# Kernel optimization log

Hardware: AMD Instinct MI355X
Metric: run time of the kernel (lower is better)

## Reference

```python
import jax, jax.numpy as jnp
import numpy as np

EMBED_DIM = 2048
NUM_HEADS = 16
HEAD_DIM = EMBED_DIM // NUM_HEADS  # 128
BLOCK_SIZE = 16
NUM_BLOCKS = 256  # max_seq_len 4096 / block_size 16
B = 64
T = 1  # single decode token per sequence (loop indexes k[i, 0, 0])


def setup_inputs() -> dict:
    key = jax.random.key(0)
    ks = jax.random.split(key, 12)
    w = 0.02
    return {
        "x": jax.random.normal(ks[0], (B, T, EMBED_DIM), jnp.float32),
        "k_cache": jax.random.normal(ks[1], (B, NUM_BLOCKS, BLOCK_SIZE, HEAD_DIM), jnp.float32),
        "v_cache": jax.random.normal(ks[2], (B, NUM_BLOCKS, BLOCK_SIZE, HEAD_DIM), jnp.float32),
        "cache_positions": jax.random.randint(ks[3], (B,), 0, NUM_BLOCKS * BLOCK_SIZE, jnp.int32),
        "Wq": jax.random.normal(ks[4], (EMBED_DIM, EMBED_DIM), jnp.float32) * w,
        "bq": jax.random.normal(ks[5], (EMBED_DIM,), jnp.float32) * w,
        "Wk": jax.random.normal(ks[6], (EMBED_DIM, HEAD_DIM), jnp.float32) * w,
        "bk": jax.random.normal(ks[7], (HEAD_DIM,), jnp.float32) * w,
        "Wv": jax.random.normal(ks[8], (EMBED_DIM, HEAD_DIM), jnp.float32) * w,
        "bv": jax.random.normal(ks[9], (HEAD_DIM,), jnp.float32) * w,
        "Wo": jax.random.normal(ks[10], (EMBED_DIM, EMBED_DIM), jnp.float32) * w,
        "bo": jax.random.normal(ks[11], (EMBED_DIM,), jnp.float32) * w,
    }


def reference(x, k_cache, v_cache, cache_positions, Wq, bq, Wk, bk, Wv, bv, Wo, bo):
    b, t, c = x.shape  # t == 1 (decode)
    hd = Wk.shape[1]
    h = c // hd
    scale = 1.0 / jnp.sqrt(jnp.asarray(hd, x.dtype))

    q = (x @ Wq + bq).reshape(b, t, h, hd)          # [B,1,H,hd]
    k_new = (x @ Wk + bk)[:, 0, :]                  # [B,hd] single KV head
    v_new = (x @ Wv + bv)[:, 0, :]                  # [B,hd]

    # Paged scatter: flatten (num_blocks, block_size) -> S slots; write new token at pos.
    s = k_cache.shape[1] * k_cache.shape[2]
    bidx = jnp.arange(b)
    kc = k_cache.reshape(b, s, hd).at[bidx, cache_positions].set(k_new)  # [B,S,hd]
    vc = v_cache.reshape(b, s, hd).at[bidx, cache_positions].set(v_new)

    # MQA: single KV head broadcast across H query heads. NOTE: softmax over the
    # FULL flattened cache (no validity mask), matching the original module.
    scores = jnp.einsum("bthd,bsd->bhts", q, kc) * scale   # [B,H,1,S]
    attn = jax.nn.softmax(scores, axis=-1)
    out = jnp.einsum("bhts,bsd->bthd", attn, vc).reshape(b, t, c)
    return out @ Wo + bo
```

## Files before the change

### kernel.cpp

```cpp
#include <hip/hip_runtime.h>
#include <math.h>

#define EMBED   2048
#define NHEADS  16
#define HD      128
#define S_TOT   4096
#define BATCH   64

typedef __attribute__((ext_vector_type(8))) short short8v;
typedef __attribute__((ext_vector_type(4))) short short4v;
typedef __attribute__((ext_vector_type(2))) short short2v;
typedef __attribute__((ext_vector_type(4))) float floatx4;

__device__ __forceinline__ unsigned short f2bf(float f) {
    unsigned u = __builtin_bit_cast(unsigned, f);
    u += 0x7fffu + ((u >> 16) & 1u);
    return (unsigned short)(u >> 16);
}

template <int CTRL>
__device__ __forceinline__ float dppf(float x) {
    int r = __builtin_amdgcn_mov_dpp(__builtin_bit_cast(int, x), CTRL, 0xF, 0xF, false);
    return __builtin_bit_cast(float, r);
}
__device__ __forceinline__ float rowmax16(float v) {
    v = fmaxf(v, dppf<0x121>(v));
    v = fmaxf(v, dppf<0x122>(v));
    v = fmaxf(v, dppf<0x124>(v));
    v = fmaxf(v, dppf<0x128>(v));
    return v;
}
__device__ __forceinline__ float rowsum16(float v) {
    v += dppf<0x121>(v);
    v += dppf<0x122>(v);
    v += dppf<0x124>(v);
    v += dppf<0x128>(v);
    return v;
}

__launch_bounds__(256)
__global__ void k1_qkv(const float* __restrict__ x,
                       const float* __restrict__ Wq, const float* __restrict__ bq,
                       const float* __restrict__ Wk, const float* __restrict__ bk,
                       const float* __restrict__ Wv, const float* __restrict__ bv,
                       float* __restrict__ qbuf, float* __restrict__ knew,
                       float* __restrict__ vnew) {
    const int tx = threadIdx.x & 31;
    const int ty = threadIdx.x >> 5;
    const int nt = blockIdx.x;
    const int kc = blockIdx.y;
    const int k0 = kc * 256;
    const int col0 = nt * 32;

    const float* W; const float* bias; float* out; int ldW;
    int cbase;
    if (col0 < 2048)       { W = Wq; bias = bq; out = qbuf; ldW = 2048; cbase = col0; }
    else if (col0 < 2176)  { W = Wk; bias = bk; out = knew; ldW = 128;  cbase = col0 - 2048; }
    else                   { W = Wv; bias = bv; out = vnew; ldW = 128;  cbase = col0 - 2176; }
    const int col = cbase + tx;

    __shared__ __align__(16) float xs[64][68];

    float acc[8] = {0, 0, 0, 0, 0, 0, 0, 0};

    for (int sub = 0; sub < 4; ++sub) {
        const int kb = k0 + sub * 64;
        #pragma unroll
        for (int i = 0; i < 4; ++i) {
            int c = threadIdx.x + i * 256;
            int r = c >> 4;
            int cc = (c & 15) << 2;
            float4 v = *(const float4*)(x + (size_t)r * EMBED + kb + cc);
            *(float4*)&xs[r][cc] = v;
        }
        __syncthreads();
        #pragma unroll
        for (int kk = 0; kk < 64; kk += 4) {
            float w0 = W[(size_t)(kb + kk + 0) * ldW + col];
            float w1 = W[(size_t)(kb + kk + 1) * ldW + col];
            float w2 = W[(size_t)(kb + kk + 2) * ldW + col];
            float w3 = W[(size_t)(kb + kk + 3) * ldW + col];
            #pragma unroll
            for (int j = 0; j < 8; ++j) {
                int m = ty + (j << 3);
                float4 xv = *(const float4*)&xs[m][kk];
                acc[j] = fmaf(xv.x, w0, acc[j]);
                acc[j] = fmaf(xv.y, w1, acc[j]);
                acc[j] = fmaf(xv.z, w2, acc[j]);
                acc[j] = fmaf(xv.w, w3, acc[j]);
            }
        }
        __syncthreads();
    }
    if (kc == 0) {
        float b = bias[col];
        #pragma unroll
        for (int j = 0; j < 8; ++j) acc[j] += b;
    }
    const int ldO = (ldW == 2048) ? 2048 : 128;
    #pragma unroll
    for (int j = 0; j < 8; ++j)
        atomicAdd(&out[(size_t)(ty + (j << 3)) * ldO + col], acc[j]);
}

__launch_bounds__(256)
__global__ void k2_attn(const float* __restrict__ qbuf,
                        const float* __restrict__ kcache,
                        const float* __restrict__ vcache,
                        const float* __restrict__ knew,
                        const float* __restrict__ vnew,
                        const int* __restrict__ cpos,
                        float* __restrict__ part_o,
                        float* __restrict__ part_ml)
{
    const int b = blockIdx.y;
    const int chunk = blockIdx.x;
    const int nch = gridDim.x;
    const int C = nch * 4;
    const int spw = S_TOT / C;
    const int nst = spw >> 5;
    const int tid = threadIdx.x;
    const int w = tid >> 6;
    const int lane = tid & 63;
    const int quad = lane >> 4;
    const int lm = lane & 15;
    const int pos = cpos[b];

    __shared__ __align__(16) short qs[16 * 136];
    __shared__ __align__(16) short vsh[4][64 * 40];
    __shared__ __align__(16) short psh[4][16 * 40];

    {
        const int h = tid >> 4, d0 = (tid & 15) << 3;
        const float* src = qbuf + (size_t)b * EMBED + h * HD + d0;
        float4 a = *(const float4*)src;
        float4 c = *(const float4*)(src + 4);
        const float s = 0.08838834764831845f;
        short8v pk;
        pk[0] = f2bf(a.x * s); pk[1] = f2bf(a.y * s);
        pk[2] = f2bf(a.z * s); pk[3] = f2bf(a.w * s);
        pk[4] = f2bf(c.x * s); pk[5] = f2bf(c.y * s);
        pk[6] = f2bf(c.z * s); pk[7] = f2bf(c.w * s);
        *(short8v*)&qs[h * 136 + d0] = pk;
    }
    __syncthreads();

    short8v aq[4];
    #pragma unroll
    for (int t = 0; t < 4; ++t)
        aq[t] = *(short8v*)&qs[lm * 136 + t * 32 + quad * 8];

    short* vt = vsh[w];
    short* pt = psh[w];

    float m_run[4] = {-INFINITY, -INFINITY, -INFINITY, -INFINITY};
    float l_run[4] = {0, 0, 0, 0};
    floatx4 oacc[8];
    #pragma unroll
    for (int i = 0; i < 8; ++i) oacc[i] = (floatx4){0, 0, 0, 0};

    const int sbase = chunk * (S_TOT / nch) + w * spw;

    for (int st = 0; st < nst; ++st) {
        const int st0 = sbase + st * 32;
        floatx4 sc2[2];
        #pragma unroll
        for (int half = 0; half < 2; ++half) {
            const int s0 = st0 + half * 16;
            const float* krow = kcache + ((size_t)b * S_TOT + s0 + lm) * HD;
            if (lm == pos - s0) krow = knew + (size_t)b * HD;
            floatx4 s = {0, 0, 0, 0};
            #pragma unroll
            for (int t = 0; t < 4; ++t) {
                float4 ka  = *(const float4*)(krow + t * 32 + quad * 8);
                float4 kb2 = *(const float4*)(krow + t * 32 + quad * 8 + 4);
                short8v bk_;
                bk_[0] = f2bf(ka.x);  bk_[1] = f2bf(ka.y);
                bk_[2] = f2bf(ka.z);  bk_[3] = f2bf(ka.w);
                bk_[4] = f2bf(kb2.x); bk_[5] = f2bf(kb2.y);
                bk_[6] = f2bf(kb2.z); bk_[7] = f2bf(kb2.w);
                s = __builtin_amdgcn_mfma_f32_16x16x32_bf16(aq[t], bk_, s, 0, 0, 0);
            }
            sc2[half] = s;
        }
        float alpha[4];
        #pragma unroll
        for (int r = 0; r < 4; ++r) {
            float mt = rowmax16(fmaxf(sc2[0][r], sc2[1][r]));
            float mn = fmaxf(m_run[r], mt);
            alpha[r] = __expf(m_run[r] - mn);
            m_run[r] = mn;
            float pA = __expf(sc2[0][r] - mn);
            float pB = __expf(sc2[1][r] - mn);
            float ss = rowsum16(pA + pB);
            l_run[r] = l_run[r] * alpha[r] + ss;
            pt[(quad * 4 + r) * 40 + lm]      = (short)f2bf(pA);
            pt[(quad * 4 + r) * 40 + 16 + lm] = (short)f2bf(pB);
        }
        #pragma unroll
        for (int dt = 0; dt < 8; ++dt) {
            oacc[dt][0] *= alpha[0]; oacc[dt][1] *= alpha[1];
            oacc[dt][2] *= alpha[2]; oacc[dt][3] *= alpha[3];
        }
        short8v ap = *(short8v*)&pt[lm * 40 + quad * 8];

        #pragma unroll
        for (int p = 0; p < 2; ++p) {
            const int sg = lane & 7;
            const int dgv = lane >> 3;
            #pragma unroll
            for (int i = 0; i < 2; ++i) {
                int dl = dgv * 4 + i * 32;
                int dglob = p * 64 + dl;
                const float* vb = vcache + ((size_t)b * S_TOT + st0 + sg * 4) * HD + dglob;
                float4 r0 = *(const float4*)(vb + 0 * HD);
                float4 r1 = *(const float4*)(vb + 1 * HD);
                float4 r2 = *(const float4*)(vb + 2 * HD);
                float4 r3 = *(const float4*)(vb + 3 * HD);
                short4v p0, p1, p2, p3;
                p0[0]=f2bf(r0.x); p0[1]=f2bf(r1.x); p0[2]=f2bf(r2.x); p0[3]=f2bf(r3.x);
                p1[0]=f2bf(r0.y); p1[1]=f2bf(r1.y); p1[2]=f2bf(r2.y); p1[3]=f2bf(r3.y);
                p2[0]=f2bf(r0.z); p2[1]=f2bf(r1.z); p2[2]=f2bf(r2.z); p2[3]=f2bf(r3.z);
                p3[0]=f2bf(r0.w); p3[1]=f2bf(r1.w); p3[2]=f2bf(r2.w); p3[3]=f2bf(r3.w);
                *(short4v*)&vt[(dl + 0) * 40 + sg * 4] = p0;
                *(short4v*)&vt[(dl + 1) * 40 + sg * 4] = p1;
                *(short4v*)&vt[(dl + 2) * 40 + sg * 4] = p2;
                *(short4v*)&vt[(dl + 3) * 40 + sg * 4] = p3;
            }
            const int prs = pos - st0;
            if (prs >= 0 && prs < 32) {
                float vvn = vnew[b * HD + p * 64 + lane];
                vt[lane * 40 + prs] = (short)f2bf(vvn);
            }
            #pragma unroll
            for (int dq = 0; dq < 4; ++dq) {
                int dt = p * 4 + dq;
                short8v bv_ = *(short8v*)&vt[(dq * 16 + lm) * 40 + quad * 8];
                oacc[dt] = __builtin_amdgcn_mfma_f32_16x16x32_bf16(ap, bv_, oacc[dt], 0, 0, 0);
            }
        }
    }

    const int cw = chunk * 4 + w;
    float* po = part_o + (size_t)(b * C + cw) * 16 * 128;
    #pragma unroll
    for (int dt = 0; dt < 8; ++dt)
        #pragma unroll
        for (int r = 0; r < 4; ++r)
            po[(quad * 4 + r) * 128 + dt * 16 + lm] = oacc[dt][r];
    if (lm < 2) {
        #pragma unroll
        for (int r = 0; r < 4; ++r) {
            float v = (lm == 0) ? m_run[r] : l_run[r];
            part_ml[((size_t)(b * C + cw) * 16 + quad * 4 + r) * 2 + lm] = v;
        }
    }
}

__launch_bounds__(128)
__global__ void k3_combine(const float* __restrict__ part_o,
                           const float* __restrict__ part_ml,
                           float* __restrict__ attn, int C) {
    const int h = blockIdx.x, b = blockIdx.y, d = threadIdx.x;
    __shared__ float sm[64], sl[64];
    if (threadIdx.x < C) {
        sm[threadIdx.x] = part_ml[((size_t)(b * C + threadIdx.x) * 16 + h) * 2 + 0];
        sl[threadIdx.x] = part_ml[((size_t)(b * C + threadIdx.x) * 16 + h) * 2 + 1];
    }
    __syncthreads();
    float M = -INFINITY;
    for (int c = 0; c < C; ++c) M = fmaxf(M, sm[c]);
    float O = 0.f, L = 0.f;
    for (int c = 0; c < C; ++c) {
        float co = __expf(sm[c] - M);
        L += co * sl[c];
        O += co * part_o[((size_t)(b * C + c) * 16 + h) * 128 + d];
    }
    attn[(size_t)b * EMBED + h * HD + d] = O / L;
}

__launch_bounds__(256)
__global__ void k4_proj(const float* __restrict__ attn,
                        const float* __restrict__ Wo, const float* __restrict__ bo,
                        float* __restrict__ out) {
    const int tx = threadIdx.x & 31;
    const int ty = threadIdx.x >> 5;
    const int col = blockIdx.x * 32 + tx;
    const int k0 = blockIdx.y * 256;

    __shared__ __align__(16) float xs[64][68];
    float acc[8] = {0, 0, 0, 0, 0, 0, 0, 0};

    for (int sub = 0; sub < 4; ++sub) {
        const int kb = k0 + sub * 64;
        #pragma unroll
        for (int i = 0; i < 4; ++i) {
            int c = threadIdx.x + i * 256;
            int r = c >> 4;
            int cc = (c & 15) << 2;
            float4 v = *(const float4*)(attn + (size_t)r * EMBED + kb + cc);
            *(float4*)&xs[r][cc] = v;
        }
        __syncthreads();
        #pragma unroll
        for (int kk = 0; kk < 64; kk += 4) {
            float w0 = Wo[(size_t)(kb + kk + 0) * EMBED + col];
            float w1 = Wo[(size_t)(kb + kk + 1) * EMBED + col];
            float w2 = Wo[(size_t)(kb + kk + 2) * EMBED + col];
            float w3 = Wo[(size_t)(kb + kk + 3) * EMBED + col];
            #pragma unroll
            for (int j = 0; j < 8; ++j) {
                int m = ty + (j << 3);
                float4 xv = *(const float4*)&xs[m][kk];
                acc[j] = fmaf(xv.x, w0, acc[j]);
                acc[j] = fmaf(xv.y, w1, acc[j]);
                acc[j] = fmaf(xv.z, w2, acc[j]);
                acc[j] = fmaf(xv.w, w3, acc[j]);
            }
        }
        __syncthreads();
    }
    if (blockIdx.y == 0) {
        float b = bo[col];
        #pragma unroll
        for (int j = 0; j < 8; ++j) acc[j] += b;
    }
    #pragma unroll
    for (int j = 0; j < 8; ++j)
        atomicAdd(&out[(size_t)(ty + (j << 3)) * EMBED + col], acc[j]);
}

extern "C" void kernel_launch(void* const* d_in, const int* in_sizes, int n_in,
                              void* d_out, int out_size, void* d_ws, size_t ws_size,
                              hipStream_t stream) {
    (void)in_sizes; (void)n_in; (void)out_size;
    const float* x  = (const float*)d_in[0];
    const float* kc = (const float*)d_in[1];
    const float* vc = (const float*)d_in[2];
    const int*   cp = (const int*)d_in[3];
    const float* Wq = (const float*)d_in[4];
    const float* bq = (const float*)d_in[5];
    const float* Wk = (const float*)d_in[6];
    const float* bk = (const float*)d_in[7];
    const float* Wv = (const float*)d_in[8];
    const float* bv = (const float*)d_in[9];
    const float* Wo = (const float*)d_in[10];
    const float* bo = (const float*)d_in[11];
    float* out = (float*)d_out;
    float* ws  = (float*)d_ws;

    float* qbuf = ws;
    float* knew = ws + 131072;
    float* vnew = ws + 139264;
    float* attn = ws + 147456;
    float* po   = ws + 278528;

    const size_t need16 = (278528ull + 64ull * 64 * 16 * 128 + 64ull * 64 * 16 * 2) * 4ull;
    const int nch = (ws_size >= need16) ? 16 : 8;
    const int C = nch * 4;
    float* pml = po + (size_t)BATCH * C * 16 * 128;

    hipMemsetAsync(qbuf, 0, 147456 * sizeof(float), stream);
    hipMemsetAsync(out, 0, (size_t)BATCH * EMBED * sizeof(float), stream);

    k1_qkv<<<dim3(72, 8), 256, 0, stream>>>(x, Wq, bq, Wk, bk, Wv, bv, qbuf, knew, vnew);
    k2_attn<<<dim3(nch, 64), 256, 0, stream>>>(qbuf, kc, vc, knew, vnew, cp, po, pml);
    k3_combine<<<dim3(16, 64), 128, 0, stream>>>(po, pml, attn, C);
    k4_proj<<<dim3(64, 8), 256, 0, stream>>>(attn, Wo, bo, out);
}
```

Measured before the change: 398.7 us.

## Load V fragments directly into MFMA registers, drop LDS transpose; fix chunk count

The attention kernel now gathers V values for each MFMA B-operand straight from global memory into registers, using strided scalar loads per lane. This replaces staging them through a transposed LDS tile, which removes the LDS writes, reads and per-wave shared buffer. The new-token V is patched in registers. The chunk count is fixed at compile time so the step loop fully unrolls, and the combine kernel now precomputes rescale factors in shared memory and uses several accumulators. The trade-off is scalar, less coalesced global loads for V, and the kernel now assumes the workspace is big enough for 16 chunks.

```diff
diff --git a/kernel.cpp b/kernel.cpp
--- a/kernel.cpp
+++ b/kernel.cpp
@@ -6,10 +6,11 @@
 #define HD      128
 #define S_TOT   4096
 #define BATCH   64
+#define NCH     16
+#define CPART   64
 
 typedef __attribute__((ext_vector_type(8))) short short8v;
 typedef __attribute__((ext_vector_type(4))) short short4v;
-typedef __attribute__((ext_vector_type(2))) short short2v;
 typedef __attribute__((ext_vector_type(4))) float floatx4;
 
 __device__ __forceinline__ unsigned short f2bf(float f) {
@@ -115,10 +116,6 @@
 {
     const int b = blockIdx.y;
     const int chunk = blockIdx.x;
-    const int nch = gridDim.x;
-    const int C = nch * 4;
-    const int spw = S_TOT / C;
-    const int nst = spw >> 5;
     const int tid = threadIdx.x;
     const int w = tid >> 6;
     const int lane = tid & 63;
@@ -127,7 +124,6 @@
     const int pos = cpos[b];
 
     __shared__ __align__(16) short qs[16 * 136];
-    __shared__ __align__(16) short vsh[4][64 * 40];
     __shared__ __align__(16) short psh[4][16 * 40];
 
     {
@@ -150,7 +146,6 @@
     for (int t = 0; t < 4; ++t)
         aq[t] = *(short8v*)&qs[lm * 136 + t * 32 + quad * 8];
 
-    short* vt = vsh[w];
     short* pt = psh[w];
 
     float m_run[4] = {-INFINITY, -INFINITY, -INFINITY, -INFINITY};
@@ -159,9 +154,10 @@
     #pragma unroll
     for (int i = 0; i < 8; ++i) oacc[i] = (floatx4){0, 0, 0, 0};
 
-    const int sbase = chunk * (S_TOT / nch) + w * spw;
-
-    for (int st = 0; st < nst; ++st) {
+    const int sbase = chunk * 256 + w * 64;
+
+    #pragma unroll
+    for (int st = 0; st < 2; ++st) {
         const int st0 = sbase + st * 32;
         floatx4 sc2[2];
         #pragma unroll
@@ -183,6 +179,28 @@
             }
             sc2[half] = s;
         }
+
+        const int prs = pos - st0;
+        short8v bvf[8];
+        #pragma unroll
+        for (int dt = 0; dt < 8; ++dt) {
+            const float* vb = vcache + ((size_t)b * S_TOT + st0 + quad * 8) * HD + dt * 16 + lm;
+            float f0 = vb[0 * HD], f1 = vb[1 * HD], f2 = vb[2 * HD], f3 = vb[3 * HD];
+            float f4 = vb[4 * HD], f5 = vb[5 * HD], f6 = vb[6 * HD], f7 = vb[7 * HD];
+            if (prs >= 0 && prs < 32) {
+                float vn = vnew[b * HD + dt * 16 + lm];
+                int jb = prs - quad * 8;
+                if (jb == 0) f0 = vn; if (jb == 1) f1 = vn;
+                if (jb == 2) f2 = vn; if (jb == 3) f3 = vn;
+                if (jb == 4) f4 = vn; if (jb == 5) f5 = vn;
+                if (jb == 6) f6 = vn; if (jb == 7) f7 = vn;
+            }
+            short8v t;
+            t[0] = f2bf(f0); t[1] = f2bf(f1); t[2] = f2bf(f2); t[3] = f2bf(f3);
+            t[4] = f2bf(f4); t[5] = f2bf(f5); t[6] = f2bf(f6); t[7] = f2bf(f7);
+            bvf[dt] = t;
+        }
+
         float alpha[4];
         #pragma unroll
         for (int r = 0; r < 4; ++r) {
@@ -205,44 +223,12 @@
         short8v ap = *(short8v*)&pt[lm * 40 + quad * 8];
 
         #pragma unroll
-        for (int p = 0; p < 2; ++p) {
-            const int sg = lane & 7;
-            const int dgv = lane >> 3;
-            #pragma unroll
-            for (int i = 0; i < 2; ++i) {
-                int dl = dgv * 4 + i * 32;
-                int dglob = p * 64 + dl;
-                const float* vb = vcache + ((size_t)b * S_TOT + st0 + sg * 4) * HD + dglob;
-                float4 r0 = *(const float4*)(vb + 0 * HD);
-                float4 r1 = *(const float4*)(vb + 1 * HD);
-                float4 r2 = *(const float4*)(vb + 2 * HD);
-                float4 r3 = *(const float4*)(vb + 3 * HD);
-                short4v p0, p1, p2, p3;
-                p0[0]=f2bf(r0.x); p0[1]=f2bf(r1.x); p0[2]=f2bf(r2.x); p0[3]=f2bf(r3.x);
-                p1[0]=f2bf(r0.y); p1[1]=f2bf(r1.y); p1[2]=f2bf(r2.y); p1[3]=f2bf(r3.y);
-                p2[0]=f2bf(r0.z); p2[1]=f2bf(r1.z); p2[2]=f2bf(r2.z); p2[3]=f2bf(r3.z);
-                p3[0]=f2bf(r0.w); p3[1]=f2bf(r1.w); p3[2]=f2bf(r2.w); p3[3]=f2bf(r3.w);
-                *(short4v*)&vt[(dl + 0) * 40 + sg * 4] = p0;
-                *(short4v*)&vt[(dl + 1) * 40 + sg * 4] = p1;
-                *(short4v*)&vt[(dl + 2) * 40 + sg * 4] = p2;
-                *(short4v*)&vt[(dl + 3) * 40 + sg * 4] = p3;
-            }
-            const int prs = pos - st0;
-            if (prs >= 0 && prs < 32) {
-                float vvn = vnew[b * HD + p * 64 + lane];
-                vt[lane * 40 + prs] = (short)f2bf(vvn);
-            }
-            #pragma unroll
-            for (int dq = 0; dq < 4; ++dq) {
-                int dt = p * 4 + dq;
-                short8v bv_ = *(short8v*)&vt[(dq * 16 + lm) * 40 + quad * 8];
-                oacc[dt] = __builtin_amdgcn_mfma_f32_16x16x32_bf16(ap, bv_, oacc[dt], 0, 0, 0);
-            }
-        }
+        for (int dt = 0; dt < 8; ++dt)
+            oacc[dt] = __builtin_amdgcn_mfma_f32_16x16x32_bf16(ap, bvf[dt], oacc[dt], 0, 0, 0);
     }
 
     const int cw = chunk * 4 + w;
-    float* po = part_o + (size_t)(b * C + cw) * 16 * 128;
+    float* po = part_o + (size_t)(b * CPART + cw) * 16 * 128;
     #pragma unroll
     for (int dt = 0; dt < 8; ++dt)
         #pragma unroll
@@ -252,7 +238,7 @@
         #pragma unroll
         for (int r = 0; r < 4; ++r) {
             float v = (lm == 0) ? m_run[r] : l_run[r];
-            part_ml[((size_t)(b * C + cw) * 16 + quad * 4 + r) * 2 + lm] = v;
+            part_ml[((size_t)(b * CPART + cw) * 16 + quad * 4 + r) * 2 + lm] = v;
         }
     }
 }
@@ -260,23 +246,33 @@
 __launch_bounds__(128)
 __global__ void k3_combine(const float* __restrict__ part_o,
                            const float* __restrict__ part_ml,
-                           float* __restrict__ attn, int C) {
+                           float* __restrict__ attn) {
     const int h = blockIdx.x, b = blockIdx.y, d = threadIdx.x;
-    __shared__ float sm[64], sl[64];
-    if (threadIdx.x < C) {
-        sm[threadIdx.x] = part_ml[((size_t)(b * C + threadIdx.x) * 16 + h) * 2 + 0];
-        sl[threadIdx.x] = part_ml[((size_t)(b * C + threadIdx.x) * 16 + h) * 2 + 1];
+    __shared__ float sm[CPART], sl[CPART], sco[CPART];
+    if (d < CPART) {
+        sm[d] = part_ml[((size_t)(b * CPART + d) * 16 + h) * 2 + 0];
+        sl[d] = part_ml[((size_t)(b * CPART + d) * 16 + h) * 2 + 1];
     }
     __syncthreads();
     float M = -INFINITY;
-    for (int c = 0; c < C; ++c) M = fmaxf(M, sm[c]);
-    float O = 0.f, L = 0.f;
-    for (int c = 0; c < C; ++c) {
-        float co = __expf(sm[c] - M);
-        L += co * sl[c];
-        O += co * part_o[((size_t)(b * C + c) * 16 + h) * 128 + d];
-    }
-    attn[(size_t)b * EMBED + h * HD + d] = O / L;
+    #pragma unroll
+    for (int c = 0; c < CPART; ++c) M = fmaxf(M, sm[c]);
+    if (d < CPART) sco[d] = __expf(sm[d] - M);
+    __syncthreads();
+    float L = 0.f;
+    #pragma unroll
+    for (int c = 0; c < CPART; ++c) L += sco[c] * sl[c];
+    float O[8] = {0, 0, 0, 0, 0, 0, 0, 0};
+    #pragma unroll
+    for (int cc = 0; cc < CPART; cc += 8) {
+        #pragma unroll
+        for (int u = 0; u < 8; ++u)
+            O[u] = fmaf(sco[cc + u],
+                        part_o[((size_t)(b * CPART + cc + u) * 16 + h) * 128 + d],
+                        O[u]);
+    }
+    float Os = ((O[0] + O[1]) + (O[2] + O[3])) + ((O[4] + O[5]) + (O[6] + O[7]));
+    attn[(size_t)b * EMBED + h * HD + d] = Os / L;
 }
 
 __launch_bounds__(256)
@@ -333,15 +329,15 @@
 extern "C" void kernel_launch(void* const* d_in, const int* in_sizes, int n_in,
                               void* d_out, int out_size, void* d_ws, size_t ws_size,
                               hipStream_t stream) {
-    (void)in_sizes; (void)n_in; (void)out_size;
+    (void)in_sizes; (void)n_in; (void)out_size; (void)ws_size;
     const float* x  = (const float*)d_in[0];
     const float* kc = (const float*)d_in[1];
     const float* vc = (const float*)d_in[2];
     const int*   cp = (const int*)d_in[3];
     const float* Wq = (const float*)d_in[4];
     const float* bq = (const float*)d_in[5];
+    const float* bk = (const float*)d_in[7];
     const float* Wk = (const float*)d_in[6];
-    const float* bk = (const float*)d_in[7];
     const float* Wv = (const float*)d_in[8];
     const float* bv = (const float*)d_in[9];
     const float* Wo = (const float*)d_in[10];
@@ -354,17 +350,13 @@
     float* vnew = ws + 139264;
     float* attn = ws + 147456;
     float* po   = ws + 278528;
-
-    const size_t need16 = (278528ull + 64ull * 64 * 16 * 128 + 64ull * 64 * 16 * 2) * 4ull;
-    const int nch = (ws_size >= need16) ? 16 : 8;
-    const int C = nch * 4;
-    float* pml = po + (size_t)BATCH * C * 16 * 128;
+    float* pml  = po + (size_t)BATCH * CPART * 16 * 128;
 
     hipMemsetAsync(qbuf, 0, 147456 * sizeof(float), stream);
     hipMemsetAsync(out, 0, (size_t)BATCH * EMBED * sizeof(float), stream);
 
     k1_qkv<<<dim3(72, 8), 256, 0, stream>>>(x, Wq, bq, Wk, bk, Wv, bv, qbuf, knew, vnew);
-    k2_attn<<<dim3(nch, 64), 256, 0, stream>>>(qbuf, kc, vc, knew, vnew, cp, po, pml);
-    k3_combine<<<dim3(16, 64), 128, 0, stream>>>(po, pml, attn, C);
+    k2_attn<<<dim3(NCH, 64), 256, 0, stream>>>(qbuf, kc, vc, knew, vnew, cp, po, pml);
+    k3_combine<<<dim3(16, 64), 128, 0, stream>>>(po, pml, attn);
     k4_proj<<<dim3(64, 8), 256, 0, stream>>>(attn, Wo, bo, out);
 }
```

Measured after the change: 395.5 us. No clear change (-0.8%).
